# Kernel tuning notes

Hardware: AMD Instinct MI355X
Metric: run time of the kernel (lower is better)

Reference implementation:

```python
import jax, jax.numpy as jnp
import numpy as np

EMBEDS = 195  # C, also used in the (unusual) 1/sqrt(C) scale


def setup_inputs() -> dict:
    key = jax.random.key(0)
    k1, k2, k3, k4 = jax.random.split(key, 4)
    B, T, C, H = 1024, 256, EMBEDS, 8
    x = jax.random.normal(k1, (B, T, C), dtype=jnp.float32)
    Wq = jax.random.normal(k2, (C, H), dtype=jnp.float32) * 0.05
    Wk = jax.random.normal(k3, (C, H), dtype=jnp.float32) * 0.05
    Wv = jax.random.normal(k4, (C, H), dtype=jnp.float32) * 0.05
    return {"x": x, "Wq": Wq, "Wk": Wk, "Wv": Wv}


def reference(x, Wq, Wk, Wv):
    B, T, C = x.shape
    q = jnp.einsum('btc,ch->bth', x, Wq)  # [B,T,H]
    k = jnp.einsum('btc,ch->bth', x, Wk)
    v = jnp.einsum('btc,ch->bth', x, Wv)
    # scores scaled by 1/sqrt(C) (embedding dim), faithful to source
    scores = jnp.einsum('bqh,bkh->bqk', q, k) * (1.0 / jnp.sqrt(jnp.float32(C)))
    causal = jnp.tril(jnp.ones((T, T), dtype=bool))  # [T,T]
    scores = jnp.where(causal, scores, -jnp.inf)
    attn = jax.nn.softmax(scores, axis=-1)
    # dropout treated as identity (eval mode) for deterministic reference
    out = jnp.einsum('bqk,bkh->bqh', attn, v)
    return out
```

## Files before the change

kernel.cpp:

```cpp
#include <hip/hip_runtime.h>
#include <hip/hip_bf16.h>
#include <stdint.h>

#define TT    256
#define CC    195
#define HH    8
#define NKT   7
#define VSTR  260
#define WSETS 14
#define WLSTR 40

typedef __attribute__((ext_vector_type(8))) short short8;
typedef __attribute__((ext_vector_type(4))) short short4v;
typedef __attribute__((ext_vector_type(4))) float f32x4;

static __device__ __forceinline__ short f2bf(float v) {
    union { __hip_bfloat16 h; short s; } cv;
    cv.h = __float2bfloat16(v);
    return cv.s;
}

__global__ __launch_bounds__(256, 4)
void fused_head(const float* __restrict__ x,
                const float* __restrict__ Wq,
                const float* __restrict__ Wk,
                const float* __restrict__ Wv,
                float* __restrict__ out)
{
    __shared__ __align__(16) short Ql[TT * 8];
    __shared__ __align__(16) short Kl[TT * 8];
    __shared__ __align__(16) short Vt[16 * VSTR];
    __shared__ __align__(16) short Wl[WSETS * 16 * WLSTR];

    const int tid  = threadIdx.x;
    const int lane = tid & 63;
    const int wv   = __builtin_amdgcn_readfirstlane(tid >> 6);
    const int b    = blockIdx.x;
    const int nn   = lane & 15;
    const int quad = lane >> 4;

    const float* __restrict__ xb = x + (size_t)b * (TT * CC);

    float xp[NKT][8];

    auto issue = [&](int ch) {
        const float* __restrict__ xrow = xb + (size_t)(ch * 64 + wv * 16 + nn) * CC;
#pragma unroll
        for (int kt = 0; kt < NKT; ++kt)
#pragma unroll
            for (int j = 0; j < 8; ++j) {
                const int k = kt * 32 + quad * 8 + j;
                xp[kt][j] = (k < CC) ? xrow[k] : 0.f;
            }
    };

    auto consume = [&](int ch) {
        const int rbase = ch * 64 + wv * 16;
        f32x4 acc0 = {0.f, 0.f, 0.f, 0.f};
        f32x4 acc1 = {0.f, 0.f, 0.f, 0.f};
#pragma unroll
        for (int kt = 0; kt < NKT; ++kt) {
            short8 a;
#pragma unroll
            for (int j = 0; j < 8; ++j) a[j] = f2bf(xp[kt][j]);
            const short8 b0 = *reinterpret_cast<const short8*>(
                Wl + ((kt * 2 + 0) * 16 + nn) * WLSTR + quad * 8);
            const short8 b1 = *reinterpret_cast<const short8*>(
                Wl + ((kt * 2 + 1) * 16 + nn) * WLSTR + quad * 8);
            acc0 = __builtin_amdgcn_mfma_f32_16x16x32_bf16(a, b0, acc0, 0, 0, 0);
            acc1 = __builtin_amdgcn_mfma_f32_16x16x32_bf16(a, b1, acc1, 0, 0, 0);
        }
#pragma unroll
        for (int r = 0; r < 4; ++r) {
            const int trow = rbase + quad * 4 + r;
            const short qs = f2bf(acc0[r]);
            if (nn < 8) {
                Ql[trow * 8 + nn] = qs;
                Vt[nn * VSTR + trow] = f2bf(acc1[r]);
            } else {
                Kl[trow * 8 + (nn - 8)] = qs;
            }
        }
    };

    const float SC2 = 0.07161149f * 1.44269504f;

    auto attn_tile = [&](int qt) {
        const int qb = qt * 16;
        const int qcol = qb + nn;

        short8 bQ = (short8){0, 0, 0, 0, 0, 0, 0, 0};
        if (quad == 0)
            bQ = *reinterpret_cast<const short8*>(Ql + (qb + nn) * 8);

        f32x4 accO = {0.f, 0.f, 0.f, 0.f};
        const int nch = (qt >> 1) + 1;
        for (int c = 0; c < nch; ++c) {
            const int kb = c * 32;
            const bool doH1 = (c < nch - 1) || (qt & 1);

            short8 aK0 = (short8){0, 0, 0, 0, 0, 0, 0, 0};
            short8 aK1 = (short8){0, 0, 0, 0, 0, 0, 0, 0};
            if (quad == 0) {
                aK0 = *reinterpret_cast<const short8*>(Kl + (kb + nn) * 8);
                if (doH1)
                    aK1 = *reinterpret_cast<const short8*>(Kl + (kb + 16 + nn) * 8);
            }
            f32x4 s0 = __builtin_amdgcn_mfma_f32_16x16x32_bf16(
                           aK0, bQ, (f32x4){0.f, 0.f, 0.f, 0.f}, 0, 0, 0);
            f32x4 s1 = {0.f, 0.f, 0.f, 0.f};
            if (doH1)
                s1 = __builtin_amdgcn_mfma_f32_16x16x32_bf16(
                         aK1, bQ, (f32x4){0.f, 0.f, 0.f, 0.f}, 0, 0, 0);

            const short* vrow = Vt + nn * VSTR + kb + quad * 4;
            const short4v v0 = *reinterpret_cast<const short4v*>(vrow);
            const short4v v1 = *reinterpret_cast<const short4v*>(vrow + 16);

            const int keyb = kb + quad * 4;
            short8 aP, bV;
#pragma unroll
            for (int r = 0; r < 4; ++r) {
                const float e0 = (keyb + r <= qcol) ? exp2f(s0[r] * SC2) : 0.f;
                const float e1 = (doH1 && (keyb + 16 + r <= qcol))
                                     ? exp2f(s1[r] * SC2) : 0.f;
                aP[r]     = f2bf(e0);
                aP[4 + r] = f2bf(e1);
                bV[r]     = v0[r];
                bV[4 + r] = v1[r];
            }
            accO = __builtin_amdgcn_mfma_f32_16x16x32_bf16(aP, bV, accO, 0, 0, 0);
        }

#pragma unroll
        for (int r = 0; r < 4; ++r) {
            const float dn = __shfl(accO[r], (lane & 48) | 8);
            if (nn < 8) {
                const int q = qb + quad * 4 + r;
                out[((size_t)b * TT + q) * HH + nn] = accO[r] / dn;
            }
        }
    };

    auto barrier_lds = [&]() {
        asm volatile("s_waitcnt lgkmcnt(0)" ::: "memory");
        __builtin_amdgcn_s_barrier();
        __builtin_amdgcn_sched_barrier(0);
    };

    issue(0);
    __builtin_amdgcn_sched_barrier(0);

    {
        uint32_t* vtw = (uint32_t*)Vt;
        const int base = (8 * VSTR) / 2;
        for (int i = tid; i < (8 * VSTR) / 2; i += 256)
            vtw[base + i] = (i < VSTR / 2) ? 0x3F803F80u : 0u;
    }
    {
        const float* Wsel0 = (nn < 8) ? (Wq + nn) : (Wk + nn - 8);
        const float* Wsel1 = Wv + (nn & 7);
        for (int set = wv; set < WSETS; set += 4) {
            const int kt = set >> 1, sv = set & 1;
            short8 frag;
#pragma unroll
            for (int j = 0; j < 8; ++j) {
                const int k = kt * 32 + quad * 8 + j;
                float v = 0.f;
                if (k < CC) {
                    if (sv == 0)        v = Wsel0[(size_t)k * HH];
                    else if (nn < 8)    v = Wsel1[(size_t)k * HH];
                }
                frag[j] = f2bf(v);
            }
            *reinterpret_cast<short8*>(Wl + (set * 16 + nn) * WLSTR + quad * 8) = frag;
        }
    }
    barrier_lds();

    consume(0);
    issue(1);
    __builtin_amdgcn_sched_barrier(0);
    barrier_lds();

    attn_tile(wv);
    consume(1);
    issue(2);
    __builtin_amdgcn_sched_barrier(0);
    barrier_lds();

    attn_tile(4 + (wv ^ 1));
    consume(2);
    issue(3);
    __builtin_amdgcn_sched_barrier(0);
    barrier_lds();

    attn_tile(8 + (wv ^ 2));
    consume(3);
    barrier_lds();

    attn_tile(12 + (wv ^ 3));
}

extern "C" void kernel_launch(void* const* d_in, const int* in_sizes, int n_in,
                              void* d_out, int out_size, void* d_ws, size_t ws_size,
                              hipStream_t stream)
{
    const float* x  = (const float*)d_in[0];
    const float* Wq = (const float*)d_in[1];
    const float* Wk = (const float*)d_in[2];
    const float* Wv = (const float*)d_in[3];
    float* out      = (float*)d_out;
    const int B = in_sizes[0] / (TT * CC);
    fused_head<<<dim3(B), dim3(256), 0, stream>>>(x, Wq, Wk, Wv, out);
}
```

Measured before the change: 297.5 us.

## Stage x chunks into LDS with async global_load_lds and keep weights in registers

```diff
diff --git a/kernel.cpp b/kernel.cpp
--- a/kernel.cpp
+++ b/kernel.cpp
@@ -7,12 +7,13 @@
 #define HH    8
 #define NKT   7
 #define VSTR  260
-#define WSETS 14
-#define WLSTR 40
 
 typedef __attribute__((ext_vector_type(8))) short short8;
 typedef __attribute__((ext_vector_type(4))) short short4v;
 typedef __attribute__((ext_vector_type(4))) float f32x4;
+
+typedef __attribute__((address_space(1))) const unsigned int g_u32;
+typedef __attribute__((address_space(3))) unsigned int l_u32;
 
 static __device__ __forceinline__ short f2bf(float v) {
     union { __hip_bfloat16 h; short s; } cv;
@@ -20,17 +21,17 @@
     return cv.s;
 }
 
-__global__ __launch_bounds__(256, 4)
+__global__ __launch_bounds__(256, 2)
 void fused_head(const float* __restrict__ x,
                 const float* __restrict__ Wq,
                 const float* __restrict__ Wk,
                 const float* __restrict__ Wv,
                 float* __restrict__ out)
 {
+    __shared__ __align__(16) float Xs[64 * CC];
     __shared__ __align__(16) short Ql[TT * 8];
     __shared__ __align__(16) short Kl[TT * 8];
     __shared__ __align__(16) short Vt[16 * VSTR];
-    __shared__ __align__(16) short Wl[WSETS * 16 * WLSTR];
 
     const int tid  = threadIdx.x;
     const int lane = tid & 63;
@@ -41,34 +42,46 @@
 
     const float* __restrict__ xb = x + (size_t)b * (TT * CC);
 
-    float xp[NKT][8];
-
     auto issue = [&](int ch) {
-        const float* __restrict__ xrow = xb + (size_t)(ch * 64 + wv * 16 + nn) * CC;
-#pragma unroll
-        for (int kt = 0; kt < NKT; ++kt)
-#pragma unroll
-            for (int j = 0; j < 8; ++j) {
-                const int k = kt * 32 + quad * 8 + j;
-                xp[kt][j] = (k < CC) ? xrow[k] : 0.f;
-            }
+        const char* src = (const char*)(xb + (size_t)ch * 64 * CC);
+        char* dst = (char*)Xs;
+        const int ubase = wv * 780;
+#pragma unroll
+        for (int j = 0; j < 13; ++j) {
+            const int u = ubase + j * 64 + lane;
+            if (j < 12 || lane < 12)
+                __builtin_amdgcn_global_load_lds(
+                    (g_u32*)(src + (size_t)u * 16),
+                    (l_u32*)(dst + (size_t)(ubase + j * 64) * 16),
+                    16, 0, 0);
+        }
     };
+
+    const float* Wsel0 = (nn < 8) ? (Wq + nn) : (Wk + nn - 8);
+    const float* Wsel1 = (nn < 8) ? (Wv + nn) : nullptr;
+    short8 Bf[NKT][2];
 
     auto consume = [&](int ch) {
         const int rbase = ch * 64 + wv * 16;
+        const float* xr = Xs + (wv * 16 + nn) * CC;
+
         f32x4 acc0 = {0.f, 0.f, 0.f, 0.f};
         f32x4 acc1 = {0.f, 0.f, 0.f, 0.f};
 #pragma unroll
-        for (int kt = 0; kt < NKT; ++kt) {
+        for (int kt = 0; kt < 6; ++kt) {
             short8 a;
 #pragma unroll
-            for (int j = 0; j < 8; ++j) a[j] = f2bf(xp[kt][j]);
-            const short8 b0 = *reinterpret_cast<const short8*>(
-                Wl + ((kt * 2 + 0) * 16 + nn) * WLSTR + quad * 8);
-            const short8 b1 = *reinterpret_cast<const short8*>(
-                Wl + ((kt * 2 + 1) * 16 + nn) * WLSTR + quad * 8);
-            acc0 = __builtin_amdgcn_mfma_f32_16x16x32_bf16(a, b0, acc0, 0, 0, 0);
-            acc1 = __builtin_amdgcn_mfma_f32_16x16x32_bf16(a, b1, acc1, 0, 0, 0);
+            for (int j = 0; j < 8; ++j)
+                a[j] = f2bf(xr[kt * 32 + quad * 8 + j]);
+            acc0 = __builtin_amdgcn_mfma_f32_16x16x32_bf16(a, Bf[kt][0], acc0, 0, 0, 0);
+            acc1 = __builtin_amdgcn_mfma_f32_16x16x32_bf16(a, Bf[kt][1], acc1, 0, 0, 0);
+        }
+        {
+            float g0 = 0.f, g1 = 0.f, g2 = 0.f;
+            if (quad == 0) { g0 = xr[192]; g1 = xr[193]; g2 = xr[194]; }
+            short8 a = (short8){f2bf(g0), f2bf(g1), f2bf(g2), 0, 0, 0, 0, 0};
+            acc0 = __builtin_amdgcn_mfma_f32_16x16x32_bf16(a, Bf[6][0], acc0, 0, 0, 0);
+            acc1 = __builtin_amdgcn_mfma_f32_16x16x32_bf16(a, Bf[6][1], acc1, 0, 0, 0);
         }
 #pragma unroll
         for (int r = 0; r < 4; ++r) {
@@ -142,12 +155,6 @@
         }
     };
 
-    auto barrier_lds = [&]() {
-        asm volatile("s_waitcnt lgkmcnt(0)" ::: "memory");
-        __builtin_amdgcn_s_barrier();
-        __builtin_amdgcn_sched_barrier(0);
-    };
-
     issue(0);
     __builtin_amdgcn_sched_barrier(0);
 
@@ -157,47 +164,54 @@
         for (int i = tid; i < (8 * VSTR) / 2; i += 256)
             vtw[base + i] = (i < VSTR / 2) ? 0x3F803F80u : 0u;
     }
-    {
-        const float* Wsel0 = (nn < 8) ? (Wq + nn) : (Wk + nn - 8);
-        const float* Wsel1 = Wv + (nn & 7);
-        for (int set = wv; set < WSETS; set += 4) {
-            const int kt = set >> 1, sv = set & 1;
-            short8 frag;
-#pragma unroll
-            for (int j = 0; j < 8; ++j) {
-                const int k = kt * 32 + quad * 8 + j;
-                float v = 0.f;
-                if (k < CC) {
-                    if (sv == 0)        v = Wsel0[(size_t)k * HH];
-                    else if (nn < 8)    v = Wsel1[(size_t)k * HH];
-                }
-                frag[j] = f2bf(v);
-            }
-            *reinterpret_cast<short8*>(Wl + (set * 16 + nn) * WLSTR + quad * 8) = frag;
+#pragma unroll
+    for (int kt = 0; kt < NKT; ++kt) {
+#pragma unroll
+        for (int j = 0; j < 8; ++j) {
+            const int k = kt * 32 + quad * 8 + j;
+            float v0 = (k < CC) ? Wsel0[(size_t)k * HH] : 0.f;
+            float v1 = (k < CC && Wsel1) ? Wsel1[(size_t)k * HH] : 0.f;
+            Bf[kt][0][j] = f2bf(v0);
+            Bf[kt][1][j] = f2bf(v1);
         }
     }
-    barrier_lds();
-
+
+    asm volatile("s_waitcnt vmcnt(0)" ::: "memory");
+    __builtin_amdgcn_sched_barrier(0);
     consume(0);
+    __builtin_amdgcn_sched_barrier(0);
     issue(1);
-    __builtin_amdgcn_sched_barrier(0);
-    barrier_lds();
+    asm volatile("s_waitcnt lgkmcnt(0)" ::: "memory");
+    __builtin_amdgcn_s_barrier();
+    __builtin_amdgcn_sched_barrier(0);
 
     attn_tile(wv);
+    asm volatile("s_waitcnt vmcnt(0)" ::: "memory");
+    __builtin_amdgcn_sched_barrier(0);
     consume(1);
+    __builtin_amdgcn_sched_barrier(0);
     issue(2);
-    __builtin_amdgcn_sched_barrier(0);
-    barrier_lds();
+    asm volatile("s_waitcnt lgkmcnt(0)" ::: "memory");
+    __builtin_amdgcn_s_barrier();
+    __builtin_amdgcn_sched_barrier(0);
 
     attn_tile(4 + (wv ^ 1));
+    asm volatile("s_waitcnt vmcnt(0)" ::: "memory");
+    __builtin_amdgcn_sched_barrier(0);
     consume(2);
+    __builtin_amdgcn_sched_barrier(0);
     issue(3);
-    __builtin_amdgcn_sched_barrier(0);
-    barrier_lds();
+    asm volatile("s_waitcnt lgkmcnt(0)" ::: "memory");
+    __builtin_amdgcn_s_barrier();
+    __builtin_amdgcn_sched_barrier(0);
 
     attn_tile(8 + (wv ^ 2));
+    asm volatile("s_waitcnt vmcnt(0)" ::: "memory");
+    __builtin_amdgcn_sched_barrier(0);
     consume(3);
-    barrier_lds();
+    asm volatile("s_waitcnt lgkmcnt(0)" ::: "memory");
+    __builtin_amdgcn_s_barrier();
+    __builtin_amdgcn_sched_barrier(0);
 
     attn_tile(12 + (wv ^ 3));
 }
```

Result: no change. 302.7 us (+1.8%).

## Split x prefetch into halves and issue weight loads before x loads

Applied to the files above, without the earlier changes.

```diff
diff --git a/kernel.cpp b/kernel.cpp
--- a/kernel.cpp
+++ b/kernel.cpp
@@ -41,28 +41,51 @@
 
     const float* __restrict__ xb = x + (size_t)b * (TT * CC);
 
-    float xp[NKT][8];
-
-    auto issue = [&](int ch) {
+    float xpA[4][8];
+    float xpB[3][8];
+
+    auto issueA = [&](int ch) {
         const float* __restrict__ xrow = xb + (size_t)(ch * 64 + wv * 16 + nn) * CC;
 #pragma unroll
-        for (int kt = 0; kt < NKT; ++kt)
+        for (int kt = 0; kt < 4; ++kt)
+#pragma unroll
+            for (int j = 0; j < 8; ++j)
+                xpA[kt][j] = xrow[kt * 32 + quad * 8 + j];
+    };
+    auto issueB = [&](int ch) {
+        const float* __restrict__ xrow = xb + (size_t)(ch * 64 + wv * 16 + nn) * CC;
+#pragma unroll
+        for (int kt = 4; kt < 7; ++kt)
 #pragma unroll
             for (int j = 0; j < 8; ++j) {
                 const int k = kt * 32 + quad * 8 + j;
-                xp[kt][j] = (k < CC) ? xrow[k] : 0.f;
-            }
-    };
-
-    auto consume = [&](int ch) {
+                xpB[kt - 4][j] = (k < CC) ? xrow[k] : 0.f;
+            }
+    };
+
+    auto consume = [&](int ch, int nxt) {
         const int rbase = ch * 64 + wv * 16;
         f32x4 acc0 = {0.f, 0.f, 0.f, 0.f};
         f32x4 acc1 = {0.f, 0.f, 0.f, 0.f};
 #pragma unroll
-        for (int kt = 0; kt < NKT; ++kt) {
+        for (int kt = 0; kt < 4; ++kt) {
             short8 a;
 #pragma unroll
-            for (int j = 0; j < 8; ++j) a[j] = f2bf(xp[kt][j]);
+            for (int j = 0; j < 8; ++j) a[j] = f2bf(xpA[kt][j]);
+            const short8 b0 = *reinterpret_cast<const short8*>(
+                Wl + ((kt * 2 + 0) * 16 + nn) * WLSTR + quad * 8);
+            const short8 b1 = *reinterpret_cast<const short8*>(
+                Wl + ((kt * 2 + 1) * 16 + nn) * WLSTR + quad * 8);
+            acc0 = __builtin_amdgcn_mfma_f32_16x16x32_bf16(a, b0, acc0, 0, 0, 0);
+            acc1 = __builtin_amdgcn_mfma_f32_16x16x32_bf16(a, b1, acc1, 0, 0, 0);
+        }
+        if (nxt >= 0) issueA(nxt);
+        __builtin_amdgcn_sched_barrier(0);
+#pragma unroll
+        for (int kt = 4; kt < 7; ++kt) {
+            short8 a;
+#pragma unroll
+            for (int j = 0; j < 8; ++j) a[j] = f2bf(xpB[kt - 4][j]);
             const short8 b0 = *reinterpret_cast<const short8*>(
                 Wl + ((kt * 2 + 0) * 16 + nn) * WLSTR + quad * 8);
             const short8 b1 = *reinterpret_cast<const short8*>(
@@ -81,6 +104,7 @@
                 Kl[trow * 8 + (nn - 8)] = qs;
             }
         }
+        if (nxt >= 0) issueB(nxt);
     };
 
     const float SC2 = 0.07161149f * 1.44269504f;
@@ -148,7 +172,26 @@
         __builtin_amdgcn_sched_barrier(0);
     };
 
-    issue(0);
+    const float* Wsel0 = (nn < 8) ? (Wq + nn) : (Wk + nn - 8);
+    const float* Wsel1 = Wv + (nn & 7);
+    float wt[4][8];
+#pragma unroll
+    for (int i = 0; i < 4; ++i) {
+        const int set = wv + i * 4;
+        const int kt = set >> 1, sv = set & 1;
+#pragma unroll
+        for (int j = 0; j < 8; ++j) {
+            const int k = kt * 32 + quad * 8 + j;
+            float v = 0.f;
+            if (set < WSETS && k < CC)
+                v = (sv == 0) ? Wsel0[(size_t)k * HH]
+                              : ((nn < 8) ? Wsel1[(size_t)k * HH] : 0.f);
+            wt[i][j] = v;
+        }
+    }
+    __builtin_amdgcn_sched_barrier(0);
+    issueA(0);
+    issueB(0);
     __builtin_amdgcn_sched_barrier(0);
 
     {
@@ -157,46 +200,31 @@
         for (int i = tid; i < (8 * VSTR) / 2; i += 256)
             vtw[base + i] = (i < VSTR / 2) ? 0x3F803F80u : 0u;
     }
-    {
-        const float* Wsel0 = (nn < 8) ? (Wq + nn) : (Wk + nn - 8);
-        const float* Wsel1 = Wv + (nn & 7);
-        for (int set = wv; set < WSETS; set += 4) {
-            const int kt = set >> 1, sv = set & 1;
+#pragma unroll
+    for (int i = 0; i < 4; ++i) {
+        const int set = wv + i * 4;
+        if (set < WSETS) {
             short8 frag;
 #pragma unroll
-            for (int j = 0; j < 8; ++j) {
-                const int k = kt * 32 + quad * 8 + j;
-                float v = 0.f;
-                if (k < CC) {
-                    if (sv == 0)        v = Wsel0[(size_t)k * HH];
-                    else if (nn < 8)    v = Wsel1[(size_t)k * HH];
-                }
-                frag[j] = f2bf(v);
-            }
+            for (int j = 0; j < 8; ++j) frag[j] = f2bf(wt[i][j]);
             *reinterpret_cast<short8*>(Wl + (set * 16 + nn) * WLSTR + quad * 8) = frag;
         }
     }
     barrier_lds();
 
-    consume(0);
-    issue(1);
-    __builtin_amdgcn_sched_barrier(0);
+    consume(0, 1);
     barrier_lds();
 
     attn_tile(wv);
-    consume(1);
-    issue(2);
-    __builtin_amdgcn_sched_barrier(0);
+    consume(1, 2);
     barrier_lds();
 
     attn_tile(4 + (wv ^ 1));
-    consume(2);
-    issue(3);
-    __builtin_amdgcn_sched_barrier(0);
+    consume(2, 3);
     barrier_lds();
 
     attn_tile(8 + (wv ^ 2));
-    consume(3);
+    consume(3, -1);
     barrier_lds();
 
     attn_tile(12 + (wv ^ 3));
```

Measured after the change: 298.7 us. About the same (+0.4%).
